# Kernel optimization log

Hardware: AMD Instinct MI355X
Metric: run time of the kernel (lower is better)

The kernel has to match this reference:

```python
import jax, jax.numpy as jnp
import numpy as np

N_CODES = 65536  # 2**(n_bits*codebook_dim) = 2**(2*8)
CB_DIM = 8


def setup_inputs() -> dict:
    key = jax.random.key(0)
    k1, k2 = jax.random.split(key)
    x = jax.random.normal(k1, (16, 2048), dtype=jnp.float32)
    codebook = jax.random.normal(k2, (N_CODES, CB_DIM), dtype=jnp.float32)
    return {"x": x, "codebook": codebook}


def reference(x, codebook):
    # per-row scaling factor (detached in torch; forward value identical)
    scale = jnp.mean(jnp.abs(x), axis=1, keepdims=True)  # [B, 1]
    u = x / scale
    flat = u.reshape(-1, codebook.shape[1])  # [M, d]

    # squared euclidean distances (argmin is identical to cdist argmin)
    d2 = (
        jnp.sum(flat * flat, axis=1, keepdims=True)
        - 2.0 * flat @ codebook.T
        + jnp.sum(codebook * codebook, axis=1)
    )  # [M, N]
    indices = jnp.argmin(d2, axis=1)  # [M]

    # EMA-style codebook replacement: cluster means with count clamp
    sums = jax.ops.segment_sum(flat, indices, num_segments=codebook.shape[0])
    counts = jax.ops.segment_sum(
        jnp.ones((flat.shape[0],), dtype=jnp.float32), indices,
        num_segments=codebook.shape[0])
    new_codebook = sums / jnp.clip(counts, 1.0, None)[:, None]

    quantized = new_codebook[indices].reshape(x.shape)
    return scale * quantized
```

## Files before the change

kernel.cpp:

```cpp
#include <hip/hip_runtime.h>
#include <stdint.h>

#define N_CODES 65536
#define CB_DIM 8
#define B_ROWS 16
#define X_COLS 2048
#define M_ROWS 4096
#define RPB 8
#define AT 512
#define NWAVE (AT / 64)

#define WS_SCALE 0
#define WS_PART  256
#define WS_SUMS  65792
#define WS_CNT   2162944

#define CODE_BODY(C0, C1, NIDX)                                            \
    {                                                                      \
        float hn = (C0).x * (C0).x;                                        \
        hn = fmaf((C0).y, (C0).y, hn);                                     \
        hn = fmaf((C0).z, (C0).z, hn);                                     \
        hn = fmaf((C0).w, (C0).w, hn);                                     \
        hn = fmaf((C1).x, (C1).x, hn);                                     \
        hn = fmaf((C1).y, (C1).y, hn);                                     \
        hn = fmaf((C1).z, (C1).z, hn);                                     \
        hn = fmaf((C1).w, (C1).w, hn);                                     \
        _Pragma("unroll")                                                  \
        for (int r = 0; r < RPB; r++) {                                    \
            float d = hn;                                                  \
            d = fmaf(nu[r * 8 + 0], (C0).x, d);                            \
            d = fmaf(nu[r * 8 + 1], (C0).y, d);                            \
            d = fmaf(nu[r * 8 + 2], (C0).z, d);                            \
            d = fmaf(nu[r * 8 + 3], (C0).w, d);                            \
            d = fmaf(nu[r * 8 + 4], (C1).x, d);                            \
            d = fmaf(nu[r * 8 + 5], (C1).y, d);                            \
            d = fmaf(nu[r * 8 + 6], (C1).z, d);                            \
            d = fmaf(nu[r * 8 + 7], (C1).w, d);                            \
            if (d < best[r]) { best[r] = d; bidx[r] = (NIDX); }            \
        }                                                                  \
    }

__global__ __launch_bounds__(256) void prep_kernel(const float* __restrict__ x,
                                                   float* __restrict__ scale_out,
                                                   float* __restrict__ nuout) {
    int tid = threadIdx.x;
    int xr = blockIdx.x;
    const float4* xv = (const float4*)(x + xr * X_COLS);
    float4 q0 = xv[tid];
    float4 q1 = xv[tid + 256];
    float s = fabsf(q0.x) + fabsf(q0.y) + fabsf(q0.z) + fabsf(q0.w)
            + fabsf(q1.x) + fabsf(q1.y) + fabsf(q1.z) + fabsf(q1.w);
    #pragma unroll
    for (int off = 32; off > 0; off >>= 1) s += __shfl_down(s, off, 64);
    __shared__ float ls[4];
    __shared__ float scale_sh;
    int wave = tid >> 6, lane = tid & 63;
    if (lane == 0) ls[wave] = s;
    __syncthreads();
    if (tid == 0) {
        float t = (ls[0] + ls[1] + ls[2] + ls[3]) * (1.0f / (float)X_COLS);
        scale_sh = t;
        scale_out[xr] = t;
    }
    __syncthreads();
    float scale = scale_sh;

    float4 n0, n1;
    n0.x = -2.0f * (q0.x / scale);  n0.y = -2.0f * (q0.y / scale);
    n0.z = -2.0f * (q0.z / scale);  n0.w = -2.0f * (q0.w / scale);
    n1.x = -2.0f * (q1.x / scale);  n1.y = -2.0f * (q1.y / scale);
    n1.z = -2.0f * (q1.z / scale);  n1.w = -2.0f * (q1.w / scale);
    float4* np = (float4*)(nuout + xr * X_COLS);
    np[tid]       = n0;
    np[tid + 256] = n1;
}

__global__ __launch_bounds__(AT, 4) void argmin_kernel(const float* __restrict__ cb,
                                                       const float* __restrict__ nuarr,
                                                       unsigned long long* __restrict__ part,
                                                       float* __restrict__ sums,
                                                       float* __restrict__ counts) {
    int tid = threadIdx.x;
    int rg  = blockIdx.x >> 1;
    int h   = blockIdx.x & 1;
    int m0  = rg * RPB;

    const float* __restrict__ up = nuarr + (size_t)m0 * CB_DIM;
    float nu[RPB * CB_DIM];
    #pragma unroll
    for (int i = 0; i < RPB * CB_DIM; i++) nu[i] = up[i];

    float best[RPB];
    int   bidx[RPB];
    #pragma unroll
    for (int r = 0; r < RPB; r++) { best[r] = 3.4e38f; bidx[r] = 0; }

    const float4* cp = (const float4*)cb;
    int n = (h << 15) + tid;
    float4 a0 = cp[2 * n],            a1 = cp[2 * n + 1];
    float4 b0 = cp[2 * (n + AT)],     b1 = cp[2 * (n + AT) + 1];
    float4 c0 = cp[2 * (n + 2 * AT)], c1 = cp[2 * (n + 2 * AT) + 1];
    float4 d0 = cp[2 * (n + 3 * AT)], d1 = cp[2 * (n + 3 * AT) + 1];

    for (int j = 0; j < 15; j++) {
        CODE_BODY(a0, a1, n)
        CODE_BODY(b0, b1, n + AT)
        a0 = cp[2 * (n + 4 * AT)]; a1 = cp[2 * (n + 4 * AT) + 1];
        b0 = cp[2 * (n + 5 * AT)]; b1 = cp[2 * (n + 5 * AT) + 1];
        CODE_BODY(c0, c1, n + 2 * AT)
        CODE_BODY(d0, d1, n + 3 * AT)
        c0 = cp[2 * (n + 6 * AT)]; c1 = cp[2 * (n + 6 * AT) + 1];
        d0 = cp[2 * (n + 7 * AT)]; d1 = cp[2 * (n + 7 * AT) + 1];
        n += 4 * AT;
    }
    CODE_BODY(a0, a1, n)
    CODE_BODY(b0, b1, n + AT)
    CODE_BODY(c0, c1, n + 2 * AT)
    CODE_BODY(d0, d1, n + 3 * AT)

    unsigned long long key[RPB];
    #pragma unroll
    for (int r = 0; r < RPB; r++) {
        unsigned int b = __float_as_uint(best[r]);
        unsigned int kk = b ^ ((unsigned int)((int)b >> 31) | 0x80000000u);
        key[r] = ((unsigned long long)kk << 32) | (unsigned int)bidx[r];
    }
    #pragma unroll
    for (int off = 32; off > 0; off >>= 1) {
        #pragma unroll
        for (int r = 0; r < RPB; r++) {
            unsigned long long o = __shfl_down(key[r], off, 64);
            if (o < key[r]) key[r] = o;
        }
    }

    __shared__ unsigned long long wred[NWAVE][RPB];
    int wave = tid >> 6, lane = tid & 63;
    if (lane == 0) {
        #pragma unroll
        for (int r = 0; r < RPB; r++) wred[wave][r] = key[r];
    }
    __syncthreads();

    if (tid < RPB) {
        unsigned long long m = wred[0][tid];
        #pragma unroll
        for (int w = 1; w < NWAVE; w++) {
            unsigned long long o = wred[w][tid];
            if (o < m) m = o;
        }
        part[(size_t)(m0 + tid) * 2 + h] = m;
        int idx = (int)(m & 0xFFFFFFFFull);
        counts[idx] = 0.f;
        float4 z = make_float4(0.f, 0.f, 0.f, 0.f);
        float4* sp = (float4*)(sums + (size_t)idx * CB_DIM);
        sp[0] = z;
        sp[1] = z;
    }
}

__global__ __launch_bounds__(256) void accum_kernel(const unsigned long long* __restrict__ part,
                                                    const float* __restrict__ nuarr,
                                                    float* __restrict__ sums,
                                                    float* __restrict__ counts) {
    int e = blockIdx.x * blockDim.x + threadIdx.x;
    int m = e >> 3, k = e & 7;
    unsigned long long k0 = part[2 * m], k1 = part[2 * m + 1];
    unsigned long long kk = k1 < k0 ? k1 : k0;
    int idx = (int)(kk & 0xFFFFFFFFull);
    if (k == 0) atomicAdd(&counts[idx], 1.0f);
    atomicAdd(&sums[(size_t)idx * CB_DIM + k], nuarr[e]);
}

__global__ __launch_bounds__(256) void gather_kernel(const unsigned long long* __restrict__ part,
                                                     const float* __restrict__ sums,
                                                     const float* __restrict__ counts,
                                                     const float* __restrict__ scale,
                                                     float* __restrict__ out) {
    int e = blockIdx.x * blockDim.x + threadIdx.x;
    int m = e >> 3, k = e & 7;
    unsigned long long k0 = part[2 * m], k1 = part[2 * m + 1];
    unsigned long long kk = k1 < k0 ? k1 : k0;
    int idx = (int)(kk & 0xFFFFFFFFull);
    float c = counts[idx];
    c = c < 1.f ? 1.f : c;
    out[e] = scale[e >> 11] * (-0.5f * (sums[(size_t)idx * CB_DIM + k] / c));
}

extern "C" void kernel_launch(void* const* d_in, const int* in_sizes, int n_in,
                              void* d_out, int out_size, void* d_ws, size_t ws_size,
                              hipStream_t stream) {
    const float* x  = (const float*)d_in[0];
    const float* cb = (const float*)d_in[1];
    char* ws = (char*)d_ws;
    float* scale   = (float*)(ws + WS_SCALE);
    unsigned long long* part = (unsigned long long*)(ws + WS_PART);
    float* sums    = (float*)(ws + WS_SUMS);
    float* counts  = (float*)(ws + WS_CNT);
    float* out     = (float*)d_out;
    float* nuarr = out;

    prep_kernel  <<<B_ROWS, 256, 0, stream>>>(x, scale, nuarr);
    argmin_kernel<<<(M_ROWS / RPB) * 2, AT, 0, stream>>>(cb, nuarr, part, sums, counts);
    accum_kernel <<<(M_ROWS * CB_DIM) / 256, 256, 0, stream>>>(part, nuarr, sums, counts);
    gather_kernel<<<(B_ROWS * X_COLS) / 256, 256, 0, stream>>>(part, sums, counts, scale, out);
}
```

Before: 139.7 us.

## Fuse scale computation into argmin kernel and search on unnormalized inputs

Removes the separate prep kernel: each argmin block recomputes its row's mean-abs scale and uses raw x against the codebook. Minimising the distance is rewritten as maximising x·c − (s/2)||c||², so no normalised buffer is materialised. The accumulation kernel divides by the scale on the fly. This saves a launch and a pass over the data, at the cost of redundant scale reductions per block and slightly different rounding in the distance comparisons.

```diff
diff --git a/kernel.cpp b/kernel.cpp
--- a/kernel.cpp
+++ b/kernel.cpp
@@ -25,58 +25,25 @@
         hn = fmaf((C1).y, (C1).y, hn);                                     \
         hn = fmaf((C1).z, (C1).z, hn);                                     \
         hn = fmaf((C1).w, (C1).w, hn);                                     \
+        float hs = hw * hn;                                                \
         _Pragma("unroll")                                                  \
         for (int r = 0; r < RPB; r++) {                                    \
-            float d = hn;                                                  \
-            d = fmaf(nu[r * 8 + 0], (C0).x, d);                            \
-            d = fmaf(nu[r * 8 + 1], (C0).y, d);                            \
-            d = fmaf(nu[r * 8 + 2], (C0).z, d);                            \
-            d = fmaf(nu[r * 8 + 3], (C0).w, d);                            \
-            d = fmaf(nu[r * 8 + 4], (C1).x, d);                            \
-            d = fmaf(nu[r * 8 + 5], (C1).y, d);                            \
-            d = fmaf(nu[r * 8 + 6], (C1).z, d);                            \
-            d = fmaf(nu[r * 8 + 7], (C1).w, d);                            \
-            if (d < best[r]) { best[r] = d; bidx[r] = (NIDX); }            \
+            float d = hs;                                                  \
+            d = fmaf(sx[r * 8 + 0], (C0).x, d);                            \
+            d = fmaf(sx[r * 8 + 1], (C0).y, d);                            \
+            d = fmaf(sx[r * 8 + 2], (C0).z, d);                            \
+            d = fmaf(sx[r * 8 + 3], (C0).w, d);                            \
+            d = fmaf(sx[r * 8 + 4], (C1).x, d);                            \
+            d = fmaf(sx[r * 8 + 5], (C1).y, d);                            \
+            d = fmaf(sx[r * 8 + 6], (C1).z, d);                            \
+            d = fmaf(sx[r * 8 + 7], (C1).w, d);                            \
+            if (d > best[r]) { best[r] = d; bidx[r] = (NIDX); }            \
         }                                                                  \
     }
 
-__global__ __launch_bounds__(256) void prep_kernel(const float* __restrict__ x,
-                                                   float* __restrict__ scale_out,
-                                                   float* __restrict__ nuout) {
-    int tid = threadIdx.x;
-    int xr = blockIdx.x;
-    const float4* xv = (const float4*)(x + xr * X_COLS);
-    float4 q0 = xv[tid];
-    float4 q1 = xv[tid + 256];
-    float s = fabsf(q0.x) + fabsf(q0.y) + fabsf(q0.z) + fabsf(q0.w)
-            + fabsf(q1.x) + fabsf(q1.y) + fabsf(q1.z) + fabsf(q1.w);
-    #pragma unroll
-    for (int off = 32; off > 0; off >>= 1) s += __shfl_down(s, off, 64);
-    __shared__ float ls[4];
-    __shared__ float scale_sh;
-    int wave = tid >> 6, lane = tid & 63;
-    if (lane == 0) ls[wave] = s;
-    __syncthreads();
-    if (tid == 0) {
-        float t = (ls[0] + ls[1] + ls[2] + ls[3]) * (1.0f / (float)X_COLS);
-        scale_sh = t;
-        scale_out[xr] = t;
-    }
-    __syncthreads();
-    float scale = scale_sh;
-
-    float4 n0, n1;
-    n0.x = -2.0f * (q0.x / scale);  n0.y = -2.0f * (q0.y / scale);
-    n0.z = -2.0f * (q0.z / scale);  n0.w = -2.0f * (q0.w / scale);
-    n1.x = -2.0f * (q1.x / scale);  n1.y = -2.0f * (q1.y / scale);
-    n1.z = -2.0f * (q1.z / scale);  n1.w = -2.0f * (q1.w / scale);
-    float4* np = (float4*)(nuout + xr * X_COLS);
-    np[tid]       = n0;
-    np[tid + 256] = n1;
-}
-
-__global__ __launch_bounds__(AT, 4) void argmin_kernel(const float* __restrict__ cb,
-                                                       const float* __restrict__ nuarr,
+__global__ __launch_bounds__(AT, 4) void argmin_kernel(const float* __restrict__ x,
+                                                       const float* __restrict__ cb,
+                                                       float* __restrict__ scale_out,
                                                        unsigned long long* __restrict__ part,
                                                        float* __restrict__ sums,
                                                        float* __restrict__ counts) {
@@ -84,16 +51,39 @@
     int rg  = blockIdx.x >> 1;
     int h   = blockIdx.x & 1;
     int m0  = rg * RPB;
+    int xr  = m0 >> 8;
 
-    const float* __restrict__ up = nuarr + (size_t)m0 * CB_DIM;
-    float nu[RPB * CB_DIM];
+    __shared__ float ls[4];
+    __shared__ float scale_sh;
+    if (tid < 256) {
+        const float4* xv = (const float4*)(x + xr * X_COLS);
+        float4 q0 = xv[tid];
+        float4 q1 = xv[tid + 256];
+        float s = fabsf(q0.x) + fabsf(q0.y) + fabsf(q0.z) + fabsf(q0.w)
+                + fabsf(q1.x) + fabsf(q1.y) + fabsf(q1.z) + fabsf(q1.w);
+        #pragma unroll
+        for (int off = 32; off > 0; off >>= 1) s += __shfl_down(s, off, 64);
+        int wave = tid >> 6, lane = tid & 63;
+        if (lane == 0) ls[wave] = s;
+    }
+    __syncthreads();
+    if (tid == 0) {
+        float t = (ls[0] + ls[1] + ls[2] + ls[3]) * (1.0f / (float)X_COLS);
+        scale_sh = t;
+        if ((blockIdx.x & 63) == 0) scale_out[xr] = t;
+    }
+    __syncthreads();
+    float hw = -0.5f * scale_sh;
+
+    const float* __restrict__ up = x + (size_t)m0 * CB_DIM;
+    float sx[RPB * CB_DIM];
     #pragma unroll
-    for (int i = 0; i < RPB * CB_DIM; i++) nu[i] = up[i];
+    for (int i = 0; i < RPB * CB_DIM; i++) sx[i] = up[i];
 
     float best[RPB];
     int   bidx[RPB];
     #pragma unroll
-    for (int r = 0; r < RPB; r++) { best[r] = 3.4e38f; bidx[r] = 0; }
+    for (int r = 0; r < RPB; r++) { best[r] = -3.4e38f; bidx[r] = 0; }
 
     const float4* cp = (const float4*)cb;
     int n = (h << 15) + tid;
@@ -123,6 +113,7 @@
     for (int r = 0; r < RPB; r++) {
         unsigned int b = __float_as_uint(best[r]);
         unsigned int kk = b ^ ((unsigned int)((int)b >> 31) | 0x80000000u);
+        kk = ~kk;
         key[r] = ((unsigned long long)kk << 32) | (unsigned int)bidx[r];
     }
     #pragma unroll
@@ -160,7 +151,8 @@
 }
 
 __global__ __launch_bounds__(256) void accum_kernel(const unsigned long long* __restrict__ part,
-                                                    const float* __restrict__ nuarr,
+                                                    const float* __restrict__ x,
+                                                    const float* __restrict__ scale,
                                                     float* __restrict__ sums,
                                                     float* __restrict__ counts) {
     int e = blockIdx.x * blockDim.x + threadIdx.x;
@@ -169,7 +161,8 @@
     unsigned long long kk = k1 < k0 ? k1 : k0;
     int idx = (int)(kk & 0xFFFFFFFFull);
     if (k == 0) atomicAdd(&counts[idx], 1.0f);
-    atomicAdd(&sums[(size_t)idx * CB_DIM + k], nuarr[e]);
+    float u = x[e] / scale[e >> 11];
+    atomicAdd(&sums[(size_t)idx * CB_DIM + k], u);
 }
 
 __global__ __launch_bounds__(256) void gather_kernel(const unsigned long long* __restrict__ part,
@@ -184,7 +177,7 @@
     int idx = (int)(kk & 0xFFFFFFFFull);
     float c = counts[idx];
     c = c < 1.f ? 1.f : c;
-    out[e] = scale[e >> 11] * (-0.5f * (sums[(size_t)idx * CB_DIM + k] / c));
+    out[e] = scale[e >> 11] * (sums[(size_t)idx * CB_DIM + k] / c);
 }
 
 extern "C" void kernel_launch(void* const* d_in, const int* in_sizes, int n_in,
@@ -198,10 +191,8 @@
     float* sums    = (float*)(ws + WS_SUMS);
     float* counts  = (float*)(ws + WS_CNT);
     float* out     = (float*)d_out;
-    float* nuarr = out;
 
-    prep_kernel  <<<B_ROWS, 256, 0, stream>>>(x, scale, nuarr);
-    argmin_kernel<<<(M_ROWS / RPB) * 2, AT, 0, stream>>>(cb, nuarr, part, sums, counts);
-    accum_kernel <<<(M_ROWS * CB_DIM) / 256, 256, 0, stream>>>(part, nuarr, sums, counts);
+    argmin_kernel<<<(M_ROWS / RPB) * 2, AT, 0, stream>>>(x, cb, scale, part, sums, counts);
+    accum_kernel <<<(M_ROWS * CB_DIM) / 256, 256, 0, stream>>>(part, x, scale, sums, counts);
     gather_kernel<<<(B_ROWS * X_COLS) / 256, 256, 0, stream>>>(part, sums, counts, scale, out);
 }
```

Result: no change. 137.7 us (-1.4%).
